# Optimization experiments

Measured on AMD Instinct MI355X. Metric: run time of the kernel, lower is better.

## Reference

```python
import jax, jax.numpy as jnp
import numpy as np

N, E, IN, H, OUT, L = 20000, 320000, 256, 256, 128, 3
EPS = 1e-5


def setup_inputs() -> dict:
    key = jax.random.key(0)
    ks = jax.random.split(key, 16)
    s = 0.02
    return {
        "x": jax.random.normal(ks[0], (N, IN), jnp.float32),
        "edge_index": jax.random.randint(ks[1], (2, E), 0, N, jnp.int64),
        "in_w": jax.random.normal(ks[2], (IN, H), jnp.float32) * s,
        "in_b": jnp.zeros((H,), jnp.float32),
        "parent_w": jax.random.normal(ks[3], (L, H, H), jnp.float32) * s,
        "child_w": jax.random.normal(ks[4], (L, H, H), jnp.float32) * s,
        "self_w": jax.random.normal(ks[5], (L, H, H), jnp.float32) * s,
        "self_b": jnp.zeros((L, H), jnp.float32),
        "ln_g": jnp.ones((L, H), jnp.float32),
        "ln_b": jnp.zeros((L, H), jnp.float32),
        "head_w1": jax.random.normal(ks[6], (H, H), jnp.float32) * s,
        "head_b1": jnp.zeros((H,), jnp.float32),
        "head_w2": jax.random.normal(ks[7], (H, OUT), jnp.float32) * s,
        "head_b2": jnp.zeros((OUT,), jnp.float32),
    }


def _aggregate(h, src, dst, weight):
    # gather -> matmul -> scatter-add -> degree-normalize
    transformed = h[src] @ weight                       # [E, H]
    agg = jax.ops.segment_sum(transformed, dst, num_segments=N)
    deg = jax.ops.segment_sum(jnp.ones((src.shape[0],), h.dtype), dst, num_segments=N)
    deg = jnp.maximum(deg, 1.0)
    return agg / deg[:, None]


def _layer_norm(x, g, b):
    mu = jnp.mean(x, axis=-1, keepdims=True)
    var = jnp.mean(jnp.square(x - mu), axis=-1, keepdims=True)
    return (x - mu) * jax.lax.rsqrt(var + EPS) * g + b


def reference(x, edge_index, in_w, in_b, parent_w, child_w, self_w, self_b,
              ln_g, ln_b, head_w1, head_b1, head_w2, head_b2):
    src, dst = edge_index[0], edge_index[1]
    h = x @ in_w + in_b                                  # input_proj
    for l in range(L):
        parent_msg = _aggregate(h, src, dst, parent_w[l])
        child_msg = _aggregate(h, dst, src, child_w[l])  # reversed edges
        out = h @ self_w[l] + self_b[l] + parent_msg + child_msg
        out = jax.nn.gelu(out, approximate=False)
        # dropout is identity in eval mode (training=False)
        h = _layer_norm(h + out, ln_g[l], ln_b[l])
    y = jax.nn.gelu(h @ head_w1 + head_b1, approximate=False)
    return y @ head_w2 + head_b2
```

## Files before the change

### kernel.cpp

```cpp
#include <hip/hip_runtime.h>


#define H 256
#define LAYERS 3
#define OUTD 128
#define LN_EPS 1e-5f

typedef short s16x8 __attribute__((ext_vector_type(8)));
typedef unsigned short u16x4 __attribute__((ext_vector_type(4)));
typedef unsigned short u16x8 __attribute__((ext_vector_type(8)));
typedef float f32x4 __attribute__((ext_vector_type(4)));

__device__ __forceinline__ unsigned short f2bf(float f) {
  unsigned int u = __float_as_uint(f);
  u += 0x7FFFu + ((u >> 16) & 1u);
  return (unsigned short)(u >> 16);
}
__device__ __forceinline__ float bf2f(unsigned short s) {
  return __uint_as_float(((unsigned int)s) << 16);
}
__device__ __forceinline__ float gelu_f(float x) {
  return 0.5f * x * (1.0f + erff(x * 0.70710678118654752440f));
}
__device__ __forceinline__ void gload16(const void* g, void* l) {
  __builtin_amdgcn_global_load_lds((const __attribute__((address_space(1))) void*)g,
                                   (__attribute__((address_space(3))) void*)l, 16, 0, 0);
}


__device__ __forceinline__ void store_split8(unsigned short* __restrict__ T, int NS, int sec,
                                             int row, int l, u16x4 hv, u16x4 lv) {
  size_t tb = ((size_t)((row >> 4) * NS + sec) << 4) + (l >> 3);
  int off = (((row & 15) + (((l >> 1) & 3) << 4)) << 3) + ((l & 1) << 2);
  *(u16x4*)(T + tb * 512 + off) = hv;
  *(u16x4*)(T + (tb + 8) * 512 + off) = lv;
}

__global__ void split_tiles_kernel(const float* __restrict__ X,
                                   unsigned short* __restrict__ T, int NS, int sec,
                                   unsigned short* __restrict__ Hc, int M)
{
  const int rb = blockIdx.x;
  const int l = threadIdx.x & 63;
  const int cq = threadIdx.x >> 6;
  const int row = (rb << 4) + (l & 15);
  if (row >= M) return;
  const float* xr = X + (size_t)row * H;
#pragma unroll
  for (int p = 0; p < 2; ++p) {
    const int c = cq + (p << 2);
    const int j0 = (c << 5) + ((l >> 4) << 3);
    f32x4 v0 = *(const f32x4*)(xr + j0);
    f32x4 v1 = *(const f32x4*)(xr + j0 + 4);
    u16x8 hv, lv;
#pragma unroll
    for (int i = 0; i < 4; ++i) {
      unsigned short hb = f2bf(v0[i]); hv[i] = hb;     lv[i] = f2bf(v0[i] - bf2f(hb));
      unsigned short hc = f2bf(v1[i]); hv[4 + i] = hc; lv[4 + i] = f2bf(v1[i] - bf2f(hc));
    }
    size_t tb = ((size_t)(rb * NS + sec) << 4);
    *(u16x8*)(T + (tb + c) * 512 + (l << 3)) = hv;
    *(u16x8*)(T + (tb + c + 8) * 512 + (l << 3)) = lv;
    if (Hc) *(u16x8*)(Hc + (size_t)row * H + j0) = hv;
  }
}

__global__ void bext_kernel(const float* __restrict__ W, unsigned short* __restrict__ Bt, int ncol) {
  int idx = blockIdx.x * 256 + threadIdx.x;
  if (idx >= H * ncol) return;
  int k = idx / ncol;
  int n = idx - k * ncol;
  float w = W[idx];
  unsigned short hb = f2bf(w);
  unsigned short lb = f2bf(w - bf2f(hb));
  size_t base = (((size_t)(n >> 4) << 4) + (k >> 5)) * 512 +
                (((n & 15) + (((k >> 3) & 3) << 4)) << 3) + (k & 7);
  Bt[base] = hb;
  Bt[base + 8 * 512] = lb;
}

__global__ void zero2_kernel(int* __restrict__ a, int* __restrict__ b, int n) {
  int i = blockIdx.x * 256 + threadIdx.x;
  if (i < n) { a[i] = 0; b[i] = 0; }
}

__global__ void deg_kernel(const int* __restrict__ src, const int* __restrict__ dst,
                           int* __restrict__ di, int* __restrict__ dox, int E) {
  int e = blockIdx.x * 256 + threadIdx.x;
  if (e >= E) return;
  atomicAdd(&dox[src[e]], 1);
  atomicAdd(&di[dst[e]], 1);
}

__global__ void rdeg_kernel(const int* __restrict__ di, const int* __restrict__ dox,
                            float* __restrict__ ri, float* __restrict__ ro, int n) {
  int i = blockIdx.x * 256 + threadIdx.x;
  if (i >= n) return;
  int a = di[i];  if (a < 1) a = 1;
  int b = dox[i]; if (b < 1) b = 1;
  ri[i] = 1.0f / (float)a;
  ro[i] = 1.0f / (float)b;
}

__global__ __launch_bounds__(1024)
void scan_kernel(const int* __restrict__ deg, int* __restrict__ rowptr, int n) {
  __shared__ int partial[1024];
  const int t = threadIdx.x;
  const int chunk = (n + 1023) / 1024;
  int b = t * chunk;
  int e = b + chunk; if (e > n) e = n;
  int s = 0;
  for (int i = b; i < e; ++i) s += deg[i];
  partial[t] = s;
  __syncthreads();
  for (int off = 1; off < 1024; off <<= 1) {
    int v = (t >= off) ? partial[t - off] : 0;
    __syncthreads();
    partial[t] += v;
    __syncthreads();
  }
  int run = (t == 0) ? 0 : partial[t - 1];
  for (int i = b; i < e; ++i) { rowptr[i] = run; run += deg[i]; }
  if (t == 1023) rowptr[n] = run;
}

__global__ void fill_kernel(const int* __restrict__ src, const int* __restrict__ dst,
                            const int* __restrict__ rp_in, const int* __restrict__ rp_out,
                            int* __restrict__ cur_in, int* __restrict__ cur_out,
                            int* __restrict__ ci_in, int* __restrict__ ci_out, int E) {
  int e = blockIdx.x * 256 + threadIdx.x;
  if (e >= E) return;
  int s = src[e], d = dst[e];
  int p = atomicAdd(&cur_in[d], 1);
  ci_in[rp_in[d] + p] = s;
  int q = atomicAdd(&cur_out[s], 1);
  ci_out[rp_out[s] + q] = d;
}

template<int NF>
__global__ __launch_bounds__(256)
void gemm_kernel(const unsigned short* __restrict__ A, int NSa,
                 const unsigned short* __restrict__ B0,
                 const unsigned short* __restrict__ B1,
                 const unsigned short* __restrict__ B2,
                 const float* __restrict__ bias, float* __restrict__ C,
                 int M, int nrb, int nsec, int do_gelu)
{
  constexpr int N = NF * 64;
  constexpr int NBT = N / 16;
  constexpr int BITER = NBT / 4;
  constexpr int SA_HI = 0, SA_LO = 2048, SB_HI = 4096;
  constexpr int SB_LO = 4096 + NBT * 512;
  __shared__ unsigned short lds[2][4096 + 2 * NBT * 512];

  const int tid = threadIdx.x;
  const int lane = tid & 63;
  const int wn = tid >> 6;
  const int m0 = blockIdx.x << 6;
  int rbw = (blockIdx.x << 2) + wn;
  if (rbw >= nrb) rbw = nrb - 1;

  f32x4 acc[4][NF] = {};

  auto STAGE = [&](int buf, int step) {
    const int s = step >> 3;
    const int c = step & 7;
    const unsigned short* Bs = (s == 0) ? B0 : ((s == 1) ? B1 : B2);
    unsigned short* base = &lds[buf][0];
    const unsigned short* pa = A + (((size_t)(rbw * NSa + s) << 4) + c) * 512 + (lane << 3);
    gload16(pa,        base + SA_HI + (wn << 9));
    gload16(pa + 4096, base + SA_LO + (wn << 9));
#pragma unroll
    for (int i = 0; i < BITER; ++i) {
      const int nb = wn + (i << 2);
      const unsigned short* pb = Bs + (((size_t)nb << 4) + c) * 512 + (lane << 3);
      gload16(pb,        base + SB_HI + (nb << 9));
      gload16(pb + 4096, base + SB_LO + (nb << 9));
    }
  };

  auto COMPUTE = [&](int buf) {
    const unsigned short* base = &lds[buf][0];
    s16x8 ah[4], al[4], bh[NF], bl[NF];
#pragma unroll
    for (int f = 0; f < 4; ++f) {
      ah[f] = *(const s16x8*)(base + SA_HI + (f << 9) + (lane << 3));
      al[f] = *(const s16x8*)(base + SA_LO + (f << 9) + (lane << 3));
    }
#pragma unroll
    for (int j = 0; j < NF; ++j) {
      const int g = wn * NF + j;
      bh[j] = *(const s16x8*)(base + SB_HI + (g << 9) + (lane << 3));
      bl[j] = *(const s16x8*)(base + SB_LO + (g << 9) + (lane << 3));
    }
#pragma unroll
    for (int i = 0; i < 4; ++i)
#pragma unroll
      for (int j = 0; j < NF; ++j)
        acc[i][j] = __builtin_amdgcn_mfma_f32_16x16x32_bf16(ah[i], bh[j], acc[i][j], 0, 0, 0);
#pragma unroll
    for (int i = 0; i < 4; ++i)
#pragma unroll
      for (int j = 0; j < NF; ++j)
        acc[i][j] = __builtin_amdgcn_mfma_f32_16x16x32_bf16(ah[i], bl[j], acc[i][j], 0, 0, 0);
#pragma unroll
    for (int i = 0; i < 4; ++i)
#pragma unroll
      for (int j = 0; j < NF; ++j)
        acc[i][j] = __builtin_amdgcn_mfma_f32_16x16x32_bf16(al[i], bh[j], acc[i][j], 0, 0, 0);
  };

  const int nsteps = nsec << 3;
  STAGE(0, 0);
  int cur = 0;
  for (int t = 0; t < nsteps - 1; ++t) {
    STAGE(cur ^ 1, t + 1);
    if (NF == 4) asm volatile("s_waitcnt vmcnt(10)" ::: "memory");
    else         asm volatile("s_waitcnt vmcnt(6)"  ::: "memory");
    __builtin_amdgcn_s_barrier();
    COMPUTE(cur);
    asm volatile("s_waitcnt lgkmcnt(0)" ::: "memory");
    __builtin_amdgcn_s_barrier();
    cur ^= 1;
  }
  asm volatile("s_waitcnt vmcnt(0)" ::: "memory");
  __builtin_amdgcn_s_barrier();
  COMPUTE(cur);

  const int r0 = (lane >> 4) << 2;
  const int cn = lane & 15;
#pragma unroll
  for (int j = 0; j < NF; ++j) {
    const int col = wn * (NF << 4) + (j << 4) + cn;
    const float bb = bias ? bias[col] : 0.0f;
#pragma unroll
    for (int i = 0; i < 4; ++i) {
      const int rowb = m0 + (i << 4) + r0;
#pragma unroll
      for (int r = 0; r < 4; ++r) {
        const int rr = rowb + r;
        if (rr < M) {
          float v = acc[i][j][r] + bb;
          if (do_gelu) v = gelu_f(v);
          C[(size_t)rr * N + col] = v;
        }
      }
    }
  }
}

__device__ __forceinline__ void gacc(const int* __restrict__ ci, int beg, int end,
                                     const unsigned short* __restrict__ Hc, int foff,
                                     int lane, int t, f32x4& acc) {
  const int lb = lane & 48;
  for (int i = beg; i < end; i += 16) {
    int cnt = end - i; if (cnt > 16) cnt = 16;
    int myidx = (t < cnt) ? ci[i + t] : 0;
    int q = 0;
    for (; q + 4 <= cnt; q += 4) {
      int id0 = __shfl(myidx, lb + q, 64);
      int id1 = __shfl(myidx, lb + q + 1, 64);
      int id2 = __shfl(myidx, lb + q + 2, 64);
      int id3 = __shfl(myidx, lb + q + 3, 64);
      u16x4 a = *(const u16x4*)(Hc + ((size_t)id0 << 8) + foff);
      u16x4 b = *(const u16x4*)(Hc + ((size_t)id1 << 8) + foff);
      u16x4 c = *(const u16x4*)(Hc + ((size_t)id2 << 8) + foff);
      u16x4 d = *(const u16x4*)(Hc + ((size_t)id3 << 8) + foff);
#pragma unroll
      for (int z = 0; z < 4; ++z)
        acc[z] += (bf2f(a[z]) + bf2f(b[z])) + (bf2f(c[z]) + bf2f(d[z]));
    }
    for (; q < cnt; ++q) {
      int id = __shfl(myidx, lb + q, 64);
      u16x4 a = *(const u16x4*)(Hc + ((size_t)id << 8) + foff);
#pragma unroll
      for (int z = 0; z < 4; ++z) acc[z] += bf2f(a[z]);
    }
  }
}

__global__ __launch_bounds__(256)
void gather_kernel(
    const int* __restrict__ rp_in, const int* __restrict__ ci_in,
    const int* __restrict__ rp_out, const int* __restrict__ ci_out,
    const float* __restrict__ ri, const float* __restrict__ ro,
    const unsigned short* __restrict__ Hc, unsigned short* __restrict__ Aext,
    int M, int nrb)
{
  __shared__ unsigned short sh[2][2][2][512];
  const int rb = blockIdx.x;
  const int s = blockIdx.y;
  const int tid = threadIdx.x;
  const int g = tid >> 4;
  const int t = tid & 15;
  const int lane = tid & 63;
  const int row = (rb << 4) + g;
  const int foff = (s << 6) + (t << 2);

  f32x4 hin = {0.f, 0.f, 0.f, 0.f}, hout = {0.f, 0.f, 0.f, 0.f};
  float wi = 0.f, wo = 0.f;
  if (row < M) {
    gacc(ci_in,  rp_in[row],  rp_in[row + 1],  Hc, foff, lane, t, hin);
    gacc(ci_out, rp_out[row], rp_out[row + 1], Hc, foff, lane, t, hout);
    wi = ri[row];
    wo = ro[row];
  }

  const int cc = t >> 3;
  const int pos = (g << 3) + (((t >> 1) & 3) << 7) + ((t & 1) << 2);
  u16x4 hv, lv;
#pragma unroll
  for (int q = 0; q < 4; ++q) {
    float v = hin[q] * wi;
    unsigned short hb = f2bf(v);
    hv[q] = hb; lv[q] = f2bf(v - bf2f(hb));
  }
  *(u16x4*)(&sh[0][0][cc][pos]) = hv;
  *(u16x4*)(&sh[0][1][cc][pos]) = lv;
#pragma unroll
  for (int q = 0; q < 4; ++q) {
    float v = hout[q] * wo;
    unsigned short hb = f2bf(v);
    hv[q] = hb; lv[q] = f2bf(v - bf2f(hb));
  }
  *(u16x4*)(&sh[1][0][cc][pos]) = hv;
  *(u16x4*)(&sh[1][1][cc][pos]) = lv;
  __syncthreads();

  const int tp = tid >> 5;
  const int sec = tp >> 2, hilo = (tp >> 1) & 1, c2 = tp & 1;
  const int cg = (s << 1) + c2 + (hilo << 3);
  size_t tile = ((size_t)(rb * 3 + 1 + sec) << 4) + cg;
  u16x8* dst = (u16x8*)(Aext + tile * 512 + ((tid & 31) << 4));
  const u16x8* srcp = (const u16x8*)(&sh[sec][hilo][c2][(tid & 31) << 4]);
  dst[0] = srcp[0];
  dst[1] = srcp[1];
}

__global__ void finalize_kernel(float* __restrict__ h, const float* __restrict__ P,
                                unsigned short* __restrict__ Aext,
                                unsigned short* __restrict__ Hc,
                                const float* __restrict__ g, const float* __restrict__ b, int M)
{
  int row = blockIdx.x * 4 + (threadIdx.x >> 6);
  if (row >= M) return;
  int l = threadIdx.x & 63;
  int j = l << 2;
  f32x4 hv = *(const f32x4*)(h + (size_t)row * H + j);
  f32x4 pv = *(const f32x4*)(P + (size_t)row * H + j);
  f32x4 t;
  float sum = 0.f, sq = 0.f;
#pragma unroll
  for (int i = 0; i < 4; ++i) {
    t[i] = hv[i] + gelu_f(pv[i]);
    sum += t[i];
    sq += t[i] * t[i];
  }
#pragma unroll
  for (int off = 1; off < 64; off <<= 1) {
    sum += __shfl_xor(sum, off, 64);
    sq  += __shfl_xor(sq, off, 64);
  }
  float mu = sum * (1.0f / H);
  float var = sq * (1.0f / H) - mu * mu;
  float rs = rsqrtf(var + LN_EPS);
  f32x4 outv;
  u16x4 hvv, lvv;
#pragma unroll
  for (int i = 0; i < 4; ++i) {
    outv[i] = (t[i] - mu) * rs * g[j + i] + b[j + i];
    unsigned short hb = f2bf(outv[i]);
    hvv[i] = hb;
    lvv[i] = f2bf(outv[i] - bf2f(hb));
  }
  *(f32x4*)(h + (size_t)row * H + j) = outv;
  *(u16x4*)(Hc + ((size_t)row << 8) + j) = hvv;
  store_split8(Aext, 3, 0, row, l, hvv, lvv);
}

extern "C" void kernel_launch(void* const* d_in, const int* in_sizes, int n_in,
                              void* d_out, int out_size, void* d_ws, size_t ws_size,
                              hipStream_t stream)
{
  const float* x        = (const float*)d_in[0];
  const int*   ei       = (const int*)d_in[1];
  const float* in_w     = (const float*)d_in[2];
  const float* in_b     = (const float*)d_in[3];
  const float* parent_w = (const float*)d_in[4];
  const float* child_w  = (const float*)d_in[5];
  const float* self_w   = (const float*)d_in[6];
  const float* self_b   = (const float*)d_in[7];
  const float* ln_g     = (const float*)d_in[8];
  const float* ln_b     = (const float*)d_in[9];
  const float* head_w1  = (const float*)d_in[10];
  const float* head_b1  = (const float*)d_in[11];
  const float* head_w2  = (const float*)d_in[12];
  const float* head_b2  = (const float*)d_in[13];

  const int M = in_sizes[0] / H;
  const int E = in_sizes[1] / 2;
  const int nrb = (M + 15) / 16;
  const int* src = ei;
  const int* dst = ei + E;

  char* w = (char*)d_ws;
  auto alloc = [&](size_t bytes) { char* p = w; w += (bytes + 255) & ~(size_t)255; return p; };
  float*          h    = (float*)alloc((size_t)M * H * 4);
  float*          P    = (float*)alloc((size_t)M * H * 4);
  unsigned short* Ax   = (unsigned short*)alloc((size_t)nrb * 16 * 512 * 2);
  unsigned short* Aext = (unsigned short*)alloc((size_t)nrb * 48 * 512 * 2);
  unsigned short* Hc   = (unsigned short*)alloc((size_t)M * H * 2);
  unsigned short* Bext = (unsigned short*)alloc((size_t)12 * H * 512 * 2);
  int*            degi = (int*)alloc((size_t)M * 4);
  int*            dego = (int*)alloc((size_t)M * 4);
  float*          ri   = (float*)alloc((size_t)M * 4);
  float*          ro   = (float*)alloc((size_t)M * 4);
  int*            rp_in   = (int*)alloc((size_t)(M + 1) * 4);
  int*            rp_out  = (int*)alloc((size_t)(M + 1) * 4);
  int*            cur_in  = (int*)alloc((size_t)M * 4);
  int*            cur_out = (int*)alloc((size_t)M * 4);
  int*            ci_in   = (int*)alloc((size_t)E * 4);
  int*            ci_out  = (int*)alloc((size_t)E * 4);
  if ((size_t)(w - (char*)d_ws) > ws_size) return;

  auto bslot = [&](int i) { return Bext + (size_t)i * H * 512; };

  bext_kernel<<<(H * H) / 256, 256, 0, stream>>>(in_w, bslot(0), H);
  for (int l = 0; l < LAYERS; ++l) {
    bext_kernel<<<(H * H) / 256, 256, 0, stream>>>(parent_w + (size_t)l * H * H, bslot(1 + l), H);
    bext_kernel<<<(H * H) / 256, 256, 0, stream>>>(child_w  + (size_t)l * H * H, bslot(4 + l), H);
    bext_kernel<<<(H * H) / 256, 256, 0, stream>>>(self_w   + (size_t)l * H * H, bslot(7 + l), H);
  }
  bext_kernel<<<(H * H) / 256, 256, 0, stream>>>(head_w1, bslot(10), H);
  bext_kernel<<<(H * OUTD) / 256, 256, 0, stream>>>(head_w2, bslot(11), OUTD);

  zero2_kernel<<<(M + 255) / 256, 256, 0, stream>>>(degi, dego, M);
  deg_kernel<<<(E + 255) / 256, 256, 0, stream>>>(src, dst, degi, dego, E);
  rdeg_kernel<<<(M + 255) / 256, 256, 0, stream>>>(degi, dego, ri, ro, M);
  scan_kernel<<<1, 1024, 0, stream>>>(degi, rp_in, M);
  scan_kernel<<<1, 1024, 0, stream>>>(dego, rp_out, M);
  zero2_kernel<<<(M + 255) / 256, 256, 0, stream>>>(cur_in, cur_out, M);
  fill_kernel<<<(E + 255) / 256, 256, 0, stream>>>(src, dst, rp_in, rp_out,
                                                   cur_in, cur_out, ci_in, ci_out, E);

  const int mb = (M + 63) / 64;
  const int ggrid = (M + 3) / 4;

  split_tiles_kernel<<<nrb, 256, 0, stream>>>(x, Ax, 1, 0, nullptr, M);
  gemm_kernel<4><<<mb, 256, 0, stream>>>(Ax, 1, bslot(0), nullptr, nullptr,
                                         in_b, h, M, nrb, 1, 0);
  split_tiles_kernel<<<nrb, 256, 0, stream>>>(h, Aext, 3, 0, Hc, M);

  for (int l = 0; l < LAYERS; ++l) {
    gather_kernel<<<dim3(nrb, 4), 256, 0, stream>>>(rp_in, ci_in, rp_out, ci_out,
                                                    ri, ro, Hc, Aext, M, nrb);
    gemm_kernel<4><<<mb, 256, 0, stream>>>(Aext, 3,
                                           bslot(7 + l), bslot(1 + l), bslot(4 + l),
                                           self_b + (size_t)l * H, P, M, nrb, 3, 0);
    finalize_kernel<<<ggrid, 256, 0, stream>>>(h, P, Aext, Hc,
                                               ln_g + (size_t)l * H, ln_b + (size_t)l * H, M);
  }

  gemm_kernel<4><<<mb, 256, 0, stream>>>(Aext, 3, bslot(10), nullptr, nullptr,
                                         head_b1, P, M, nrb, 1, 1);
  split_tiles_kernel<<<nrb, 256, 0, stream>>>(P, Ax, 1, 0, nullptr, M);
  gemm_kernel<2><<<mb, 256, 0, stream>>>(Ax, 1, bslot(11), nullptr, nullptr,
                                         head_b2, (float*)d_out, M, nrb, 1, 0);
}
```

Measured before the change: 535.8 us.

## Map gather feature slices to XCDs and load neighbor indices directly

Result: no change. 539.4 us (+0.7%).

```diff
diff --git a/kernel.cpp b/kernel.cpp
--- a/kernel.cpp
+++ b/kernel.cpp
@@ -251,31 +251,23 @@
 
 __device__ __forceinline__ void gacc(const int* __restrict__ ci, int beg, int end,
                                      const unsigned short* __restrict__ Hc, int foff,
-                                     int lane, int t, f32x4& acc) {
-  const int lb = lane & 48;
-  for (int i = beg; i < end; i += 16) {
-    int cnt = end - i; if (cnt > 16) cnt = 16;
-    int myidx = (t < cnt) ? ci[i + t] : 0;
-    int q = 0;
-    for (; q + 4 <= cnt; q += 4) {
-      int id0 = __shfl(myidx, lb + q, 64);
-      int id1 = __shfl(myidx, lb + q + 1, 64);
-      int id2 = __shfl(myidx, lb + q + 2, 64);
-      int id3 = __shfl(myidx, lb + q + 3, 64);
-      u16x4 a = *(const u16x4*)(Hc + ((size_t)id0 << 8) + foff);
-      u16x4 b = *(const u16x4*)(Hc + ((size_t)id1 << 8) + foff);
-      u16x4 c = *(const u16x4*)(Hc + ((size_t)id2 << 8) + foff);
-      u16x4 d = *(const u16x4*)(Hc + ((size_t)id3 << 8) + foff);
-#pragma unroll
-      for (int z = 0; z < 4; ++z)
-        acc[z] += (bf2f(a[z]) + bf2f(b[z])) + (bf2f(c[z]) + bf2f(d[z]));
-    }
-    for (; q < cnt; ++q) {
-      int id = __shfl(myidx, lb + q, 64);
-      u16x4 a = *(const u16x4*)(Hc + ((size_t)id << 8) + foff);
-#pragma unroll
-      for (int z = 0; z < 4; ++z) acc[z] += bf2f(a[z]);
-    }
+                                     f32x4& acc) {
+  int i = beg;
+  for (; i + 4 <= end; i += 4) {
+    int id0 = ci[i], id1 = ci[i + 1], id2 = ci[i + 2], id3 = ci[i + 3];
+    u16x4 a = *(const u16x4*)(Hc + ((size_t)id0 << 8) + foff);
+    u16x4 b = *(const u16x4*)(Hc + ((size_t)id1 << 8) + foff);
+    u16x4 c = *(const u16x4*)(Hc + ((size_t)id2 << 8) + foff);
+    u16x4 d = *(const u16x4*)(Hc + ((size_t)id3 << 8) + foff);
+#pragma unroll
+    for (int z = 0; z < 4; ++z)
+      acc[z] += (bf2f(a[z]) + bf2f(b[z])) + (bf2f(c[z]) + bf2f(d[z]));
+  }
+  for (; i < end; ++i) {
+    int id = ci[i];
+    u16x4 a = *(const u16x4*)(Hc + ((size_t)id << 8) + foff);
+#pragma unroll
+    for (int z = 0; z < 4; ++z) acc[z] += bf2f(a[z]);
   }
 }
 
@@ -288,20 +280,22 @@
     int M, int nrb)
 {
   __shared__ unsigned short sh[2][2][2][512];
-  const int rb = blockIdx.x;
-  const int s = blockIdx.y;
+  const int b = blockIdx.x;
+  const int xcd = b & 7;
+  const int s = xcd >> 1;
+  const int rb = ((b >> 3) << 1) + (xcd & 1);
+  if (rb >= nrb) return;
   const int tid = threadIdx.x;
   const int g = tid >> 4;
   const int t = tid & 15;
-  const int lane = tid & 63;
   const int row = (rb << 4) + g;
   const int foff = (s << 6) + (t << 2);
 
   f32x4 hin = {0.f, 0.f, 0.f, 0.f}, hout = {0.f, 0.f, 0.f, 0.f};
   float wi = 0.f, wo = 0.f;
   if (row < M) {
-    gacc(ci_in,  rp_in[row],  rp_in[row + 1],  Hc, foff, lane, t, hin);
-    gacc(ci_out, rp_out[row], rp_out[row + 1], Hc, foff, lane, t, hout);
+    gacc(ci_in,  rp_in[row],  rp_in[row + 1],  Hc, foff, hin);
+    gacc(ci_out, rp_out[row], rp_out[row + 1], Hc, foff, hout);
     wi = ri[row];
     wo = ro[row];
   }
@@ -445,6 +439,7 @@
 
   const int mb = (M + 63) / 64;
   const int ggrid = (M + 3) / 4;
+  const int xgrid = 8 * ((nrb + 1) / 2);
 
   split_tiles_kernel<<<nrb, 256, 0, stream>>>(x, Ax, 1, 0, nullptr, M);
   gemm_kernel<4><<<mb, 256, 0, stream>>>(Ax, 1, bslot(0), nullptr, nullptr,
@@ -452,8 +447,8 @@
   split_tiles_kernel<<<nrb, 256, 0, stream>>>(h, Aext, 3, 0, Hc, M);
 
   for (int l = 0; l < LAYERS; ++l) {
-    gather_kernel<<<dim3(nrb, 4), 256, 0, stream>>>(rp_in, ci_in, rp_out, ci_out,
-                                                    ri, ro, Hc, Aext, M, nrb);
+    gather_kernel<<<xgrid, 256, 0, stream>>>(rp_in, ci_in, rp_out, ci_out,
+                                             ri, ro, Hc, Aext, M, nrb);
     gemm_kernel<4><<<mb, 256, 0, stream>>>(Aext, 3,
                                            bslot(7 + l), bslot(1 + l), bslot(4 + l),
                                            self_b + (size_t)l * H, P, M, nrb, 3, 0);
```
